# Kernel tuning notes

Hardware: AMD Instinct MI355X
Metric: run time of the kernel (lower is better)

The kernel has to match this reference:

```python
import jax, jax.numpy as jnp
import numpy as np

B, MQ, MK = 8, 512, 2048
Q_DIM, KV_DIM = 1024, 256
H = 8
QKC, VC = 1024, 1024
DQ, DV = QKC // H, VC // H
EPS = 1e-5  # nn.LayerNorm default


def _layer_norm(x, w, b):
    m = jnp.mean(x, axis=-1, keepdims=True)
    v = jnp.var(x, axis=-1, keepdims=True)
    return (x - m) * jax.lax.rsqrt(v + EPS) * w + b


def setup_inputs() -> dict:
    key = jax.random.key(0)
    ks = jax.random.split(key, 12)
    hidden_states = jax.random.normal(ks[0], (B, MQ, Q_DIM), dtype=jnp.float32)
    inputs = jax.random.normal(ks[1], (B, MK, KV_DIM), dtype=jnp.float32)
    # ragged per-batch kv lengths -> prefix-valid mask (matches keys[i, :n] packing)
    lengths = jax.random.randint(ks[2], (B,), MK // 4, MK + 1)
    inputs_mask = (jnp.arange(MK)[None, :] < lengths[:, None]).astype(jnp.int32)
    s = 0.02
    return {
        "hidden_states": hidden_states,
        "inputs": inputs,
        "inputs_mask": inputs_mask,
        "ln1_w": jnp.ones((Q_DIM,), jnp.float32),
        "ln1_b": jnp.zeros((Q_DIM,), jnp.float32),
        "ln2_w": jnp.ones((KV_DIM,), jnp.float32),
        "ln2_b": jnp.zeros((KV_DIM,), jnp.float32),
        "Wq": s * jax.random.normal(ks[3], (Q_DIM, QKC), dtype=jnp.float32),
        "bq": jnp.zeros((QKC,), jnp.float32),
        "Wk": s * jax.random.normal(ks[4], (KV_DIM, QKC), dtype=jnp.float32),
        "bk": jnp.zeros((QKC,), jnp.float32),
        "Wv": s * jax.random.normal(ks[5], (KV_DIM, VC), dtype=jnp.float32),
        "bv": jnp.zeros((VC,), jnp.float32),
    }


def reference(hidden_states, inputs, inputs_mask, ln1_w, ln1_b, ln2_w, ln2_b,
              Wq, bq, Wk, bk, Wv, bv):
    hs = _layer_norm(hidden_states, ln1_w, ln1_b)      # [B, MQ, Q_DIM]
    kv = _layer_norm(inputs, ln2_w, ln2_b)             # [B, MK, KV_DIM]

    q = (hs @ Wq + bq).reshape(B, MQ, H, DQ)           # [B, MQ, H, DQ]
    k = (kv @ Wk + bk).reshape(B, MK, H, DQ)           # [B, MK, H, DQ]
    v = (kv @ Wv + bv).reshape(B, MK, H, DV)           # [B, MK, H, DV]

    scores = jnp.einsum("bqhd,bkhd->bhqk", q, k) / jnp.sqrt(jnp.float32(DQ))
    mask_f = inputs_mask.astype(scores.dtype)          # [B, MK]
    neg = jnp.finfo(scores.dtype).min
    scores = scores + (1.0 - mask_f)[:, None, None, :] * neg
    probs = jax.nn.softmax(scores, axis=-1)            # [B, H, MQ, MK]

    ctx = jnp.einsum("bhqk,bkhd->bqhd", probs, v)      # [B, MQ, H, DV]
    return ctx.reshape(B, MQ, H * DV)
```

## Files before the change

kernel.cpp:

```cpp
#include <hip/hip_runtime.h>

#define DI __device__ __forceinline__

typedef _Float16 f16x8 __attribute__((ext_vector_type(8)));
typedef _Float16 f16x4 __attribute__((ext_vector_type(4)));
typedef float    f32x4 __attribute__((ext_vector_type(4)));

namespace {

constexpr int kB  = 8;
constexpr int kMQ = 512;
constexpr int kMK = 2048;
constexpr int kQKC = 1024;
constexpr int kVC  = 1024;

DI void gload16(const void* g, void* l) {
  __builtin_amdgcn_global_load_lds(
      (const __attribute__((address_space(1))) void*)g,
      (__attribute__((address_space(3))) void*)l, 16, 0, 0);
}

DI f32x4 mfma16(f16x8 a, f16x8 b, f32x4 c) {
  return __builtin_amdgcn_mfma_f32_16x16x32_f16(a, b, c, 0, 0, 0);
}

DI f32x4 mfma16k16(f16x4 a, f16x4 b, f32x4 c) {
  return __builtin_amdgcn_mfma_f32_16x16x16f16(a, b, c, 0, 0, 0);
}

template<int K, int N>
DI void transpose_dev(const float* __restrict__ W, _Float16* __restrict__ WT,
                      int bid, float (*t)[65]) {
  int nt = bid % (N / 64), kt = bid / (N / 64);
  int k0 = kt * 64, n0 = nt * 64;
  int tid = threadIdx.x;
#pragma unroll
  for (int j = 0; j < 16; ++j) {
    int e = tid + j * 256;
    int r = e >> 6, c = e & 63;
    t[r][c] = W[(size_t)(k0 + r) * N + n0 + c];
  }
  __syncthreads();
#pragma unroll
  for (int j = 0; j < 16; ++j) {
    int e = tid + j * 256;
    int r = e >> 6, c = e & 63;
    WT[(size_t)(n0 + r) * K + k0 + c] = (_Float16)t[c][r];
  }
}

DI void ln1024_dev(const float* __restrict__ x, const float* __restrict__ w,
                   const float* __restrict__ bb, _Float16* __restrict__ y,
                   int row, float* red) {
  int tid = threadIdx.x;
  const float4* xr = (const float4*)(x + (size_t)row * 1024);
  float4 v = xr[tid];
  float s = v.x + v.y + v.z + v.w;
  float q = v.x * v.x + v.y * v.y + v.z * v.z + v.w * v.w;
#pragma unroll
  for (int m = 32; m; m >>= 1) { s += __shfl_xor(s, m); q += __shfl_xor(q, m); }
  if ((tid & 63) == 0) { red[tid >> 6] = s; red[4 + (tid >> 6)] = q; }
  __syncthreads();
  s = red[0] + red[1] + red[2] + red[3];
  q = red[4] + red[5] + red[6] + red[7];
  float mean = s * (1.0f / 1024.0f);
  float var = q * (1.0f / 1024.0f) - mean * mean;
  float inv = rsqrtf(var + 1e-5f);
  f16x4 o;
  const float* wp = w + tid * 4;
  const float* bp = bb + tid * 4;
  o[0] = (_Float16)((v.x - mean) * inv * wp[0] + bp[0]);
  o[1] = (_Float16)((v.y - mean) * inv * wp[1] + bp[1]);
  o[2] = (_Float16)((v.z - mean) * inv * wp[2] + bp[2]);
  o[3] = (_Float16)((v.w - mean) * inv * wp[3] + bp[3]);
  *(f16x4*)(y + (size_t)row * 1024 + tid * 4) = o;
}

DI void ln256_dev(const float* __restrict__ x, const float* __restrict__ w,
                  const float* __restrict__ bb, _Float16* __restrict__ y, int bid) {
  int tid = threadIdx.x;
  int lane = tid & 63, wv = tid >> 6;
  size_t row = (size_t)bid * 4 + wv;
  const float4* xr = (const float4*)(x + row * 256);
  float4 v = xr[lane];
  float s = v.x + v.y + v.z + v.w;
  float q = v.x * v.x + v.y * v.y + v.z * v.z + v.w * v.w;
#pragma unroll
  for (int m = 32; m; m >>= 1) { s += __shfl_xor(s, m); q += __shfl_xor(q, m); }
  float mean = s * (1.0f / 256.0f);
  float var = q * (1.0f / 256.0f) - mean * mean;
  float inv = rsqrtf(var + 1e-5f);
  f16x4 o;
  const float* wp = w + lane * 4;
  const float* bp = bb + lane * 4;
  o[0] = (_Float16)((v.x - mean) * inv * wp[0] + bp[0]);
  o[1] = (_Float16)((v.y - mean) * inv * wp[1] + bp[1]);
  o[2] = (_Float16)((v.z - mean) * inv * wp[2] + bp[2]);
  o[3] = (_Float16)((v.w - mean) * inv * wp[3] + bp[3]);
  *(f16x4*)(y + row * 256 + lane * 4) = o;
}

__global__ __launch_bounds__(256) void prep_all(
    const float* __restrict__ Wq, const float* __restrict__ Wk, const float* __restrict__ Wv,
    _Float16* __restrict__ WqT, _Float16* __restrict__ WkT, _Float16* __restrict__ WvT,
    const float* __restrict__ hs, const float* __restrict__ ln1w, const float* __restrict__ ln1b,
    _Float16* __restrict__ hsln,
    const float* __restrict__ xin, const float* __restrict__ ln2w, const float* __restrict__ ln2b,
    _Float16* __restrict__ kvln) {
  __shared__ float tbuf[64][65];
  int bid = blockIdx.x;
  if (bid < 256) {
    transpose_dev<1024, 1024>(Wq, WqT, bid, tbuf);
  } else if (bid < 320) {
    transpose_dev<256, 1024>(Wk, WkT, bid - 256, tbuf);
  } else if (bid < 384) {
    transpose_dev<256, 1024>(Wv, WvT, bid - 320, tbuf);
  } else if (bid < 4480) {
    ln1024_dev(hs, ln1w, ln1b, hsln, bid - 384, (float*)tbuf);
  } else {
    ln256_dev(xin, ln2w, ln2b, kvln, bid - 4480);
  }
}

template<int M, int N, int K, bool BIAS_ROW, int MMODE>
DI void gemm_dev(const _Float16* __restrict__ A, const _Float16* __restrict__ Bt,
                 const float* __restrict__ bias, const int* __restrict__ msk,
                 _Float16* __restrict__ C, int bid,
                 _Float16 (*As)[128 * 64], _Float16 (*Bs)[128 * 64]) {
  int tid = threadIdx.x, lane = tid & 63;
  int w = tid >> 6, wr = w >> 1, wc = w & 1;
  constexpr int NT = N / 128;
  constexpr int KT = K / 64;
  int mt = bid / NT, nt = bid % NT;
  if constexpr (MMODE == 1) { if (msk[mt * 128] == 0) return; }
  if constexpr (MMODE == 2) { if (msk[nt * 128] == 0) return; }
  const int l15 = lane & 15, l4 = lane >> 4;

  f32x4 acc[4][4] = {};

  const int rS = tid >> 3;
  const int cpS = tid & 7;

  auto stage = [&](int kt, int bufi) {
#pragma unroll
    for (int j = 0; j < 4; ++j) {
      int rr = rS + j * 32;
      int cg = cpS ^ (rr & 7);
      gload16(A  + ((size_t)(mt * 128 + rr) * K + kt * 64 + cg * 8),
              (char*)As[bufi] + j * 4096 + tid * 16);
      gload16(Bt + ((size_t)(nt * 128 + rr) * K + kt * 64 + cg * 8),
              (char*)Bs[bufi] + j * 4096 + tid * 16);
    }
  };

  stage(0, 0);
  __syncthreads();

  for (int kt = 0; kt < KT; ++kt) {
    int cur = kt & 1;
    if (kt + 1 < KT) stage(kt + 1, cur ^ 1);
#pragma unroll
    for (int ss = 0; ss < 2; ++ss) {
      f16x8 a[4], b[4];
#pragma unroll
      for (int m = 0; m < 4; ++m) {
        int ra = wr * 64 + m * 16 + l15;
        int cl = ss * 4 + l4;
        a[m] = *(const f16x8*)((const char*)As[cur] + ra * 128 + ((cl ^ (ra & 7)) << 4));
        int rb = wc * 64 + m * 16 + l15;
        b[m] = *(const f16x8*)((const char*)Bs[cur] + rb * 128 + ((cl ^ (rb & 7)) << 4));
      }
#pragma unroll
      for (int m = 0; m < 4; ++m)
#pragma unroll
        for (int n = 0; n < 4; ++n)
          acc[m][n] = mfma16(a[m], b[n], acc[m][n]);
    }
    __syncthreads();
  }

#pragma unroll
  for (int m = 0; m < 4; ++m) {
#pragma unroll
    for (int n = 0; n < 4; ++n) {
      int gi0 = mt * 128 + wr * 64 + m * 16 + l4 * 4;
      int gj  = nt * 128 + wc * 64 + n * 16 + l15;
#pragma unroll
      for (int r = 0; r < 4; ++r) {
        int gi = gi0 + r;
        float v = acc[m][n][r] + (BIAS_ROW ? bias[gi] : bias[gj]);
        C[(size_t)gi * N + gj] = (_Float16)v;
      }
    }
  }
}

__global__ __launch_bounds__(256) void gemm_all(
    const _Float16* __restrict__ hsln, const _Float16* __restrict__ WqT,
    const float* __restrict__ bq, _Float16* __restrict__ qbf,
    const _Float16* __restrict__ kvln, const _Float16* __restrict__ WkT,
    const float* __restrict__ bk, _Float16* __restrict__ kbf,
    const _Float16* __restrict__ WvT, const float* __restrict__ bv,
    _Float16* __restrict__ vT, const int* __restrict__ msk) {
  __shared__ _Float16 As[2][128 * 64];
  __shared__ _Float16 Bs[2][128 * 64];
  int bid = blockIdx.x;
  if (bid < 256) {
    gemm_dev<4096, 1024, 1024, false, 0>(hsln, WqT, bq, nullptr, qbf, bid, As, Bs);
  } else if (bid < 1280) {
    gemm_dev<16384, 1024, 256, false, 1>(kvln, WkT, bk, msk, kbf, bid - 256, As, Bs);
  } else {
    gemm_dev<1024, 16384, 256, true, 2>(WvT, kvln, bv, msk, vT, bid - 1280, As, Bs);
  }
}

__global__ __launch_bounds__(256, 2) void attn_kernel(const _Float16* __restrict__ qm,
                                                      const _Float16* __restrict__ km,
                                                      const _Float16* __restrict__ vT,
                                                      const int* __restrict__ msk,
                                                      float* __restrict__ out) {
  __shared__ _Float16 Ks[2][64 * 128];
  __shared__ _Float16 Vst[2][128 * 64];

  int tid = threadIdx.x, lane = tid & 63, w = tid >> 6;
  int bh = blockIdx.x & 63, qt = blockIdx.x >> 6;
  int h = bh & 7, b = bh >> 3;
  const int l15 = lane & 15, l4 = lane >> 4;

  int vld = (lane < 32) ? msk[b * kMK + lane * 64] : 0;
  int ntiles = __popcll(__ballot(vld != 0));
  int lv = msk[b * kMK + (ntiles - 1) * 64 + lane];
  int lastlen = __popcll(__ballot(lv != 0));

  f16x8 qf[4];
#pragma unroll
  for (int kc = 0; kc < 4; ++kc)
    qf[kc] = *(const f16x8*)(qm +
        (size_t)(b * kMQ + qt * 64 + w * 16 + l15) * kQKC +
        h * 128 + kc * 32 + l4 * 8);

  f32x4 o[8] = {};
  float rm = -1e30f, rl = 0.0f;

  const float sl2 = 0.08838834764831845f * 1.4426950408889634f;

  const int rK = tid >> 4, cpK = tid & 15;
  const int rV = tid >> 3, cpV = tid & 7;

  auto stage = [&](int kt, int bufi) {
#pragma unroll
    for (int j = 0; j < 4; ++j) {
      int rr = rK + j * 16;
      int cg = cpK ^ (rr & 7);
      gload16(km + (size_t)(b * kMK + kt * 64 + rr) * kQKC + h * 128 + cg * 8,
              (char*)Ks[bufi] + j * 4096 + tid * 16);
    }
#pragma unroll
    for (int j = 0; j < 4; ++j) {
      int dv = rV + j * 32;
      int cg = cpV ^ (dv & 7);
      gload16(vT + (size_t)(h * 128 + dv) * (kB * kMK) + (size_t)b * kMK + kt * 64 + cg * 8,
              (char*)Vst[bufi] + j * 4096 + tid * 16);
    }
  };

  stage(0, 0);
  __syncthreads();

  for (int kt = 0; kt < ntiles; ++kt) {
    int cur = kt & 1;
    if (kt + 1 < ntiles) stage(kt + 1, cur ^ 1);

    f32x4 sc[4] = {};
    __builtin_amdgcn_s_setprio(1);
#pragma unroll
    for (int kc = 0; kc < 4; ++kc) {
      f16x8 kb[4];
#pragma unroll
      for (int kf = 0; kf < 4; ++kf) {
        int rr = kf * 16 + l15;
        int cl = kc * 4 + l4;
        kb[kf] = *(const f16x8*)((const char*)Ks[cur] + rr * 256 + ((cl ^ (rr & 7)) << 4));
      }
#pragma unroll
      for (int kf = 0; kf < 4; ++kf)
        sc[kf] = mfma16(kb[kf], qf[kc], sc[kf]);
    }
    __builtin_amdgcn_s_setprio(0);

    if (kt == ntiles - 1) {
#pragma unroll
      for (int kf = 0; kf < 4; ++kf)
#pragma unroll
        for (int r = 0; r < 4; ++r)
          if (kf * 16 + l4 * 4 + r >= lastlen) sc[kf][r] = -3e38f;
    }

    float mx = sc[0][0];
#pragma unroll
    for (int kf = 0; kf < 4; ++kf)
#pragma unroll
      for (int r = 0; r < 4; ++r) mx = fmaxf(mx, sc[kf][r]);
    mx = fmaxf(mx, __shfl_xor(mx, 16));
    mx = fmaxf(mx, __shfl_xor(mx, 32));
    float al = 1.0f;
    if (__any(mx > rm)) {
      float nm = fmaxf(rm, mx);
      al = __builtin_amdgcn_exp2f((rm - nm) * sl2);
      rm = nm;
#pragma unroll
      for (int n = 0; n < 8; ++n)
#pragma unroll
        for (int r = 0; r < 4; ++r) o[n][r] *= al;
    }
    float nms = rm * sl2;
    float ts = 0.0f;
#pragma unroll
    for (int kf = 0; kf < 4; ++kf)
#pragma unroll
      for (int r = 0; r < 4; ++r) {
        float p = __builtin_amdgcn_exp2f(sc[kf][r] * sl2 - nms);
        sc[kf][r] = p;
        ts += p;
      }
    ts += __shfl_xor(ts, 16);
    ts += __shfl_xor(ts, 32);
    rl = rl * al + ts;

    f16x4 pb[4];
#pragma unroll
    for (int kf = 0; kf < 4; ++kf)
#pragma unroll
      for (int r = 0; r < 4; ++r) pb[kf][r] = (_Float16)sc[kf][r];

    __builtin_amdgcn_s_setprio(1);
#pragma unroll
    for (int n = 0; n < 8; ++n) {
      int dv = n * 16 + l15;
#pragma unroll
      for (int kf = 0; kf < 4; ++kf) {
        int phys = (kf * 2 + (l4 >> 1)) ^ (l15 & 7);
        f16x4 vb = *(const f16x4*)((const char*)Vst[cur] +
                                   dv * 128 + (phys << 4) + (l4 & 1) * 8);
        o[n] = mfma16k16(vb, pb[kf], o[n]);
      }
    }
    __builtin_amdgcn_s_setprio(0);
    __syncthreads();
  }

  float inv = 1.0f / rl;
  int qg = qt * 64 + w * 16 + l15;
#pragma unroll
  for (int n = 0; n < 8; ++n) {
    f32x4 ov;
#pragma unroll
    for (int r = 0; r < 4; ++r) ov[r] = o[n][r] * inv;
    *(f32x4*)(out + ((size_t)b * kMQ + qg) * kVC + h * 128 + n * 16 + l4 * 4) = ov;
  }
}

}

extern "C" void kernel_launch(void* const* d_in, const int* in_sizes, int n_in,
                              void* d_out, int out_size, void* d_ws, size_t ws_size,
                              hipStream_t stream) {
  (void)in_sizes; (void)n_in; (void)out_size; (void)ws_size;
  const float* hs   = (const float*)d_in[0];
  const float* xin  = (const float*)d_in[1];
  const int*   msk  = (const int*)d_in[2];
  const float* ln1w = (const float*)d_in[3];
  const float* ln1b = (const float*)d_in[4];
  const float* ln2w = (const float*)d_in[5];
  const float* ln2b = (const float*)d_in[6];
  const float* Wq   = (const float*)d_in[7];
  const float* bq   = (const float*)d_in[8];
  const float* Wk   = (const float*)d_in[9];
  const float* bk   = (const float*)d_in[10];
  const float* Wv   = (const float*)d_in[11];
  const float* bv   = (const float*)d_in[12];
  float* out = (float*)d_out;

  char* ws = (char*)d_ws;
  _Float16* qbf  = (_Float16*)(ws + 0);
  _Float16* kbf  = (_Float16*)(ws + 8388608);
  _Float16* vT   = (_Float16*)(ws + 41943040);
  _Float16* hsln = (_Float16*)(ws + 75497472);
  _Float16* kvln = (_Float16*)(ws + 83886080);
  _Float16* WqT  = (_Float16*)(ws + 92274688);
  _Float16* WkT  = (_Float16*)(ws + 94371840);
  _Float16* WvT  = (_Float16*)(ws + 94896128);

  prep_all<<<8576, 256, 0, stream>>>(Wq, Wk, Wv, WqT, WkT, WvT,
                                     hs, ln1w, ln1b, hsln,
                                     xin, ln2w, ln2b, kvln);
  gemm_all<<<2304, 256, 0, stream>>>(hsln, WqT, bq, qbf,
                                     kvln, WkT, bk, kbf,
                                     WvT, bv, vT, msk);
  attn_kernel<<<512, 256, 0, stream>>>(qbf, kbf, vT, msk, out);
}
```

Measured before the change: 120.2 us.

## Split attention KV range in two halves with combine pass and length-sorted scheduling

Splits each attention (batch, head, q-tile) work item into two halves over the valid KV tiles, doubling the grid from 512 to 1024 blocks. Partial fp16 outputs and running max/sum are written to reused workspace buffers, and a new combine kernel merges them with rescaling. A schedule table built in the prep kernel orders work items so the longest batches launch first. The aim is better CU occupancy and load balance on ragged lengths, at the cost of an extra launch, extra partial-result traffic and fp16 rounding of the partial outputs.

New measurement: 123.0 us. +2.3%, slower.

```diff
diff --git a/kernel.cpp b/kernel.cpp
--- a/kernel.cpp
+++ b/kernel.cpp
@@ -106,7 +106,8 @@
     const float* __restrict__ hs, const float* __restrict__ ln1w, const float* __restrict__ ln1b,
     _Float16* __restrict__ hsln,
     const float* __restrict__ xin, const float* __restrict__ ln2w, const float* __restrict__ ln2b,
-    _Float16* __restrict__ kvln) {
+    _Float16* __restrict__ kvln,
+    const int* __restrict__ msk, int* __restrict__ work) {
   __shared__ float tbuf[64][65];
   int bid = blockIdx.x;
   if (bid < 256) {
@@ -117,8 +118,39 @@
     transpose_dev<256, 1024>(Wv, WvT, bid - 320, tbuf);
   } else if (bid < 4480) {
     ln1024_dev(hs, ln1w, ln1b, hsln, bid - 384, (float*)tbuf);
+  } else if (bid < 8576) {
+    ln256_dev(xin, ln2w, ln2b, kvln, bid - 4480);
   } else {
-    ln256_dev(xin, ln2w, ln2b, kvln, bid - 4480);
+    int* wbuf = (int*)tbuf;
+    int t = threadIdx.x;
+    int b = t >> 5, tile = t & 31;
+    wbuf[t] = (msk[b * kMK + tile * 64] != 0) ? 1 : 0;
+    __syncthreads();
+    if (t < 8) {
+      int s = 0;
+      for (int i = 0; i < 32; ++i) s += wbuf[t * 32 + i];
+      wbuf[256 + t] = s;
+    }
+    __syncthreads();
+    if (t == 0) {
+      int ord[8];
+      for (int i = 0; i < 8; ++i) ord[i] = i;
+      for (int i = 1; i < 8; ++i) {
+        int o = ord[i], j = i;
+        while (j > 0 && wbuf[256 + ord[j - 1]] < wbuf[256 + o]) { ord[j] = ord[j - 1]; --j; }
+        ord[j] = o;
+      }
+      for (int i = 0; i < 8; ++i) wbuf[264 + i] = ord[i];
+    }
+    __syncthreads();
+#pragma unroll
+    for (int k = 0; k < 4; ++k) {
+      int p = t + k * 256;
+      int s = p >> 7, h = p & 7, qh = (p >> 3) & 15;
+      int qt = qh >> 1, half = qh & 1;
+      int bb = wbuf[264 + s];
+      work[p] = (bb * 8 + h) | (qt << 6) | (half << 9);
+    }
   }
 }
 
@@ -218,12 +250,15 @@
                                                       const _Float16* __restrict__ km,
                                                       const _Float16* __restrict__ vT,
                                                       const int* __restrict__ msk,
-                                                      float* __restrict__ out) {
+                                                      const int* __restrict__ work,
+                                                      _Float16* __restrict__ pO,
+                                                      float* __restrict__ pML) {
   __shared__ _Float16 Ks[2][64 * 128];
   __shared__ _Float16 Vst[2][128 * 64];
 
   int tid = threadIdx.x, lane = tid & 63, w = tid >> 6;
-  int bh = blockIdx.x & 63, qt = blockIdx.x >> 6;
+  int v = work[blockIdx.x];
+  int bh = v & 63, qt = (v >> 6) & 7, half = (v >> 9) & 1;
   int h = bh & 7, b = bh >> 3;
   const int l15 = lane & 15, l4 = lane >> 4;
 
@@ -231,6 +266,10 @@
   int ntiles = __popcll(__ballot(vld != 0));
   int lv = msk[b * kMK + (ntiles - 1) * 64 + lane];
   int lastlen = __popcll(__ballot(lv != 0));
+
+  int h1 = (ntiles + 1) >> 1;
+  int t0 = half ? h1 : 0;
+  int t1 = half ? ntiles : h1;
 
   f16x8 qf[4];
 #pragma unroll
@@ -264,12 +303,12 @@
     }
   };
 
-  stage(0, 0);
+  stage(t0, 0);
   __syncthreads();
 
-  for (int kt = 0; kt < ntiles; ++kt) {
-    int cur = kt & 1;
-    if (kt + 1 < ntiles) stage(kt + 1, cur ^ 1);
+  for (int kt = t0; kt < t1; ++kt) {
+    int cur = (kt - t0) & 1;
+    if (kt + 1 < t1) stage(kt + 1, cur ^ 1);
 
     f32x4 sc[4] = {};
     __builtin_amdgcn_s_setprio(1);
@@ -349,14 +388,57 @@
     __syncthreads();
   }
 
-  float inv = 1.0f / rl;
-  int qg = qt * 64 + w * 16 + l15;
+  int item = bh * 16 + qt * 2 + half;
+  _Float16* po = pO + (size_t)item * 8192;
+  int qr = w * 16 + l15;
 #pragma unroll
   for (int n = 0; n < 8; ++n) {
-    f32x4 ov;
-#pragma unroll
-    for (int r = 0; r < 4; ++r) ov[r] = o[n][r] * inv;
-    *(f32x4*)(out + ((size_t)b * kMQ + qg) * kVC + h * 128 + n * 16 + l4 * 4) = ov;
+    f16x4 st;
+#pragma unroll
+    for (int r = 0; r < 4; ++r) st[r] = (_Float16)o[n][r];
+    *(f16x4*)(po + qr * 128 + n * 16 + l4 * 4) = st;
+  }
+  if (l4 == 0) {
+    pML[(item * 64 + qr) * 2 + 0] = rm;
+    pML[(item * 64 + qr) * 2 + 1] = rl;
+  }
+}
+
+__global__ __launch_bounds__(256) void combine_kernel(const _Float16* __restrict__ pO,
+                                                      const float* __restrict__ pML,
+                                                      float* __restrict__ out) {
+  int cid = blockIdx.x;
+  int bh = cid & 63, qt = cid >> 6;
+  int h = bh & 7, b = bh >> 3;
+  int t = threadIdx.x;
+  int q = t >> 2, c = t & 3;
+  const float sl2 = 0.08838834764831845f * 1.4426950408889634f;
+
+  int i1 = bh * 16 + qt * 2, i2 = i1 + 1;
+  float m1 = pML[(i1 * 64 + q) * 2 + 0], l1 = pML[(i1 * 64 + q) * 2 + 1];
+  float m2 = pML[(i2 * 64 + q) * 2 + 0], l2 = pML[(i2 * 64 + q) * 2 + 1];
+  float m = fmaxf(m1, m2);
+  float w1 = __builtin_amdgcn_exp2f((m1 - m) * sl2);
+  float w2 = __builtin_amdgcn_exp2f((m2 - m) * sl2);
+  float inv = 1.0f / (l1 * w1 + l2 * w2);
+  w1 *= inv; w2 *= inv;
+
+  const _Float16* p1 = pO + (size_t)i1 * 8192 + q * 128;
+  const _Float16* p2 = pO + (size_t)i2 * 8192 + q * 128;
+  float* orow = out + ((size_t)b * kMQ + qt * 64 + q) * kVC + h * 128;
+#pragma unroll
+  for (int j = 0; j < 4; ++j) {
+    int col = c * 32 + j * 8;
+    f16x8 a = *(const f16x8*)(p1 + col);
+    f16x8 bb = *(const f16x8*)(p2 + col);
+    f32x4 o0, o1;
+#pragma unroll
+    for (int r = 0; r < 4; ++r) {
+      o0[r] = (float)a[r] * w1 + (float)bb[r] * w2;
+      o1[r] = (float)a[4 + r] * w1 + (float)bb[4 + r] * w2;
+    }
+    *(f32x4*)(orow + col) = o0;
+    *(f32x4*)(orow + col + 4) = o1;
   }
 }
 
@@ -390,12 +472,17 @@
   _Float16* WqT  = (_Float16*)(ws + 92274688);
   _Float16* WkT  = (_Float16*)(ws + 94371840);
   _Float16* WvT  = (_Float16*)(ws + 94896128);
-
-  prep_all<<<8576, 256, 0, stream>>>(Wq, Wk, Wv, WqT, WkT, WvT,
+  int*      work = (int*)(ws + 95420416);
+  _Float16* pO   = hsln;
+  float*    pML  = (float*)WqT;
+
+  prep_all<<<8577, 256, 0, stream>>>(Wq, Wk, Wv, WqT, WkT, WvT,
                                      hs, ln1w, ln1b, hsln,
-                                     xin, ln2w, ln2b, kvln);
+                                     xin, ln2w, ln2b, kvln,
+                                     msk, work);
   gemm_all<<<2304, 256, 0, stream>>>(hsln, WqT, bq, qbf,
                                      kvln, WkT, bk, kbf,
                                      WvT, bv, vT, msk);
-  attn_kernel<<<512, 256, 0, stream>>>(qbf, kbf, vT, msk, out);
-}
+  attn_kernel<<<1024, 256, 0, stream>>>(qbf, kbf, vT, msk, work, pO, pML);
+  combine_kernel<<<512, 256, 0, stream>>>(pO, pML, out);
+}
```
